# Kernel optimization log

Hardware: AMD Instinct MI355X
Metric: run time of the kernel (lower is better)

Reference implementation:

```python
import jax, jax.numpy as jnp
import numpy as np

EMB = 1024
E = 8        # num_experts
TOPK = 2
HID = 2048   # expert_dim

def setup_inputs() -> dict:
    key = jax.random.key(0)
    ks = jax.random.split(key, 10)
    s = lambda fan_in: 1.0 / np.sqrt(fan_in)
    x  = jax.random.normal(ks[0], (2, 2048, EMB), dtype=jnp.float32)
    Wr = jax.random.normal(ks[1], (EMB, E), dtype=jnp.float32) * s(EMB)
    br = jnp.zeros((E,), dtype=jnp.float32)
    # stacked expert weights, stored (in, out) so y = x @ W + b
    W1 = jax.random.normal(ks[2], (E, EMB, HID), dtype=jnp.float32) * s(EMB)
    b1 = jax.random.normal(ks[3], (E, HID), dtype=jnp.float32) * 0.01
    Wg = jax.random.normal(ks[4], (E, HID, HID), dtype=jnp.float32) * s(HID)
    bg = jax.random.normal(ks[5], (E, HID), dtype=jnp.float32) * 0.01
    W2 = jax.random.normal(ks[6], (E, HID, EMB), dtype=jnp.float32) * s(HID)
    b2 = jax.random.normal(ks[7], (E, EMB), dtype=jnp.float32) * 0.01
    return {"x": x, "Wr": Wr, "br": br, "W1": W1, "b1": b1,
            "Wg": Wg, "bg": bg, "W2": W2, "b2": b2}

def reference(x, Wr, br, W1, b1, Wg, bg, W2, b2):
    B, S, D = x.shape
    xt = x.reshape(B * S, D)                                  # [T, D]
    logits = xt @ Wr + br                                     # [T, E]
    probs = jax.nn.softmax(logits, axis=-1)
    topk_p, topk_i = jax.lax.top_k(probs, TOPK)               # [T, K]
    # dense gate matrix (top-k probs, NOT renormalized, as in source)
    gates = jnp.sum(jax.nn.one_hot(topk_i, E, dtype=xt.dtype) * topk_p[..., None], axis=1)  # [T, E]
    # expert MLP: layer1 (no act) -> relu(linear) -> layer2, for all experts
    h = jnp.einsum('td,edh->teh', xt, W1) + b1                # [T, E, HID]
    h = jax.nn.relu(jnp.einsum('teh,ehg->teg', h, Wg) + bg)   # [T, E, HID]
    y = jnp.einsum('teh,ehd->ted', h, W2) + b2                # [T, E, D]
    out = jnp.einsum('te,ted->td', gates, y)                  # weighted combine
    return out.reshape(B, S, D)
```

## Files before the change

kernel.cpp:

```cpp
#include <hip/hip_runtime.h>
#include <hip/hip_bf16.h>
#include <stdint.h>

#define NTOK 4096
#define EMBD 1024
#define NEXP 8
#define HIDD 2048
#define NPAIR (NTOK * 2)

typedef __attribute__((ext_vector_type(8))) __bf16 bf16x8;
typedef __attribute__((ext_vector_type(4))) float f32x4;

union V16 { uint4 u; bf16x8 b; };

__device__ __forceinline__ uint16_t f2bf(float f) {
    uint32_t u = __float_as_uint(f);
    return (uint16_t)((u + 0x7FFFu + ((u >> 16) & 1u)) >> 16);
}

__global__ __launch_bounds__(256) void cast_x_kernel(const float* __restrict__ x,
                                                     uint16_t* __restrict__ xb) {
    int i = blockIdx.x * 256 + threadIdx.x;
    float4 v = ((const float4*)x)[i];
    ushort4 o;
    o.x = f2bf(v.x); o.y = f2bf(v.y); o.z = f2bf(v.z); o.w = f2bf(v.w);
    ((ushort4*)xb)[i] = o;
}

__global__ __launch_bounds__(64) void router_kernel(const float* __restrict__ x,
                                                    const float* __restrict__ Wr,
                                                    const float* __restrict__ br,
                                                    int* __restrict__ counts,
                                                    int* __restrict__ pair_e,
                                                    float* __restrict__ pair_p) {
    int tok = blockIdx.x;
    int lane = threadIdx.x;
    const float* xr = x + (size_t)tok * EMBD;
    float acc[NEXP];
#pragma unroll
    for (int e = 0; e < NEXP; e++) acc[e] = 0.f;
    for (int d = lane; d < EMBD; d += 64) {
        float xv = xr[d];
#pragma unroll
        for (int e = 0; e < NEXP; e++) acc[e] += xv * Wr[d * NEXP + e];
    }
#pragma unroll
    for (int e = 0; e < NEXP; e++) {
#pragma unroll
        for (int off = 32; off > 0; off >>= 1)
            acc[e] += __shfl_down(acc[e], off, 64);
    }
    if (lane == 0) {
        float lg[NEXP];
#pragma unroll
        for (int e = 0; e < NEXP; e++) lg[e] = acc[e] + br[e];
        int e0 = 0;
#pragma unroll
        for (int e = 1; e < NEXP; e++) if (lg[e] > lg[e0]) e0 = e;
        int e1 = (e0 == 0) ? 1 : 0;
#pragma unroll
        for (int e = 0; e < NEXP; e++) if (e != e0 && lg[e] > lg[e1]) e1 = e;
        float mx = lg[0];
#pragma unroll
        for (int e = 1; e < NEXP; e++) mx = fmaxf(mx, lg[e]);
        float s = 0.f, p[NEXP];
#pragma unroll
        for (int e = 0; e < NEXP; e++) { p[e] = __expf(lg[e] - mx); s += p[e]; }
        float inv = 1.f / s;
        pair_e[tok * 2 + 0] = e0; pair_p[tok * 2 + 0] = p[e0] * inv;
        pair_e[tok * 2 + 1] = e1; pair_p[tok * 2 + 1] = p[e1] * inv;
        atomicAdd(&counts[e0], 1);
        atomicAdd(&counts[e1], 1);
    }
}

__global__ void scan_kernel(const int* __restrict__ counts, int* __restrict__ offsets) {
    if (threadIdx.x == 0 && blockIdx.x == 0) {
        int s = 0;
        for (int e = 0; e < NEXP; e++) { offsets[e] = s; s += counts[e]; }
    }
}

__global__ __launch_bounds__(256) void scatter_kernel(const int* __restrict__ pair_e,
                                                      const float* __restrict__ pair_p,
                                                      const int* __restrict__ offsets,
                                                      int* __restrict__ cursors,
                                                      int* __restrict__ toklist,
                                                      float* __restrict__ problist) {
    int i = blockIdx.x * 256 + threadIdx.x;
    int e = pair_e[i];
    int pos = offsets[e] + atomicAdd(&cursors[e], 1);
    toklist[pos] = i >> 1;
    problist[pos] = pair_p[i];
}

template <int KDIM, int NDIM, bool GATHER_A, bool RELU, bool SCATTER>
__global__ __launch_bounds__(256) void gemm_kernel(
    const uint16_t* __restrict__ Abase, const float* __restrict__ Wbase,
    const float* __restrict__ bbase, uint16_t* __restrict__ Obf,
    float* __restrict__ Oscat, const int* __restrict__ counts,
    const int* __restrict__ offsets, const int* __restrict__ toklist,
    const float* __restrict__ problist) {
    int e = blockIdx.z;
    int n_e = counts[e];
    int m0 = blockIdx.y * 64;
    if (m0 >= n_e) return;
    int n0 = blockIdx.x * 64;
    int offs = offsets[e];
    const float* W = Wbase + (size_t)e * KDIM * NDIM;
    const float* bias = bbase + (size_t)e * NDIM;

    __shared__ uint16_t As[64][40];
    __shared__ uint16_t Bs[64][40];

    int tid = threadIdx.x;
    int lane = tid & 63;
    int wave = tid >> 6;
    int wm = (wave >> 1) * 32, wn = (wave & 1) * 32;
    int qd = lane >> 4;
    int l16 = lane & 15;

    int ar = tid >> 2;
    int aseg = (tid & 3) * 8;
    bool avalid = (m0 + ar) < n_e;
    int arow;
    if (GATHER_A) {
        int p = offs + m0 + (avalid ? ar : 0);
        arow = toklist[p];
    } else {
        arow = offs + m0 + (avalid ? ar : 0);
    }
    const uint16_t* Arow = Abase + (size_t)arow * KDIM + aseg;

    int bn = tid & 63;
    int bkg = (tid >> 6) * 8;

    f32x4 acc[2][2];
    f32x4 zero = {0.f, 0.f, 0.f, 0.f};
    acc[0][0] = zero; acc[0][1] = zero; acc[1][0] = zero; acc[1][1] = zero;

    for (int kb = 0; kb < KDIM; kb += 32) {
        uint4 av = {0u, 0u, 0u, 0u};
        if (avalid) av = *(const uint4*)(Arow + kb);
        *(uint4*)(&As[ar][aseg]) = av;
#pragma unroll
        for (int kk = 0; kk < 8; kk++) {
            float bv = W[(size_t)(kb + bkg + kk) * NDIM + n0 + bn];
            Bs[bn][bkg + kk] = f2bf(bv);
        }
        __syncthreads();
        V16 afr[2], bfr[2];
#pragma unroll
        for (int t = 0; t < 2; t++) {
            afr[t].u = *(const uint4*)(&As[wm + t * 16 + l16][qd * 8]);
            bfr[t].u = *(const uint4*)(&Bs[wn + t * 16 + l16][qd * 8]);
        }
#pragma unroll
        for (int ti = 0; ti < 2; ti++)
#pragma unroll
            for (int tj = 0; tj < 2; tj++)
                acc[ti][tj] = __builtin_amdgcn_mfma_f32_16x16x32_bf16(
                    afr[ti].b, bfr[tj].b, acc[ti][tj], 0, 0, 0);
        __syncthreads();
    }

#pragma unroll
    for (int ti = 0; ti < 2; ti++) {
        int rbase = m0 + wm + ti * 16 + qd * 4;
#pragma unroll
        for (int tj = 0; tj < 2; tj++) {
            int col = n0 + wn + tj * 16 + l16;
            float bv = bias[col];
#pragma unroll
            for (int r = 0; r < 4; r++) {
                int row = rbase + r;
                if (row < n_e) {
                    float v = acc[ti][tj][r] + bv;
                    if (RELU) v = fmaxf(v, 0.f);
                    if (SCATTER) {
                        int p = offs + row;
                        int tok = toklist[p];
                        float pr = problist[p];
                        atomicAdd(&Oscat[(size_t)tok * NDIM + col], pr * v);
                    } else {
                        Obf[(size_t)(offs + row) * NDIM + col] = f2bf(v);
                    }
                }
            }
        }
    }
}

extern "C" void kernel_launch(void* const* d_in, const int* in_sizes, int n_in,
                              void* d_out, int out_size, void* d_ws, size_t ws_size,
                              hipStream_t stream) {
    const float* x  = (const float*)d_in[0];
    const float* Wr = (const float*)d_in[1];
    const float* br = (const float*)d_in[2];
    const float* W1 = (const float*)d_in[3];
    const float* b1 = (const float*)d_in[4];
    const float* Wg = (const float*)d_in[5];
    const float* bg = (const float*)d_in[6];
    const float* W2 = (const float*)d_in[7];
    const float* b2 = (const float*)d_in[8];
    float* out = (float*)d_out;

    char* ws = (char*)d_ws;
    uint16_t* xb = (uint16_t*)ws;
    uint16_t* h  = (uint16_t*)(ws + (8ull << 20));
    uint16_t* g  = (uint16_t*)(ws + (40ull << 20));
    int* meta = (int*)(ws + (72ull << 20));
    int*   counts   = meta;
    int*   offsets  = meta + 8;
    int*   cursors  = meta + 16;
    int*   pair_e   = meta + 24;
    int*   toklist  = meta + 24 + NPAIR;
    float* pair_p   = (float*)(meta + 24 + 2 * NPAIR);
    float* problist = (float*)(meta + 24 + 3 * NPAIR);

    hipMemsetAsync(out, 0, (size_t)NTOK * EMBD * sizeof(float), stream);
    hipMemsetAsync(counts, 0, 24 * sizeof(int), stream);

    cast_x_kernel<<<(NTOK * EMBD) / (256 * 4), 256, 0, stream>>>(x, xb);
    router_kernel<<<NTOK, 64, 0, stream>>>(x, Wr, br, counts, pair_e, pair_p);
    scan_kernel<<<1, 64, 0, stream>>>(counts, offsets);
    scatter_kernel<<<NPAIR / 256, 256, 0, stream>>>(pair_e, pair_p, offsets, cursors,
                                                    toklist, problist);
    gemm_kernel<EMBD, HIDD, true, false, false>
        <<<dim3(HIDD / 64, NTOK / 64, NEXP), 256, 0, stream>>>(
            xb, W1, b1, h, nullptr, counts, offsets, toklist, problist);
    gemm_kernel<HIDD, HIDD, false, true, false>
        <<<dim3(HIDD / 64, NTOK / 64, NEXP), 256, 0, stream>>>(
            h, Wg, bg, g, nullptr, counts, offsets, toklist, problist);
    gemm_kernel<HIDD, EMBD, false, false, true>
        <<<dim3(EMBD / 64, NTOK / 64, NEXP), 256, 0, stream>>>(
            g, W2, b2, nullptr, out, counts, offsets, toklist, problist);
}
```

Baseline: 858.9 us.

## Pre-transpose weights to bf16, enlarge GEMM tiles, use direct LDS loads, replace atomics with combine

Adds a transcast kernel that converts each expert's weights to bf16 in transposed (N,K) layout, so the GEMM B loads become contiguous 16-byte global_load_lds transfers into XOR-swizzled shared memory. GEMM tiles grow from 64x64 to 128x128, with 4x4 MFMA tiles per wave for more reuse. The last GEMM writes bf16 per-pair outputs, and a separate combine kernel does the weighted sum per token, replacing the fp32 atomicAdd scatter and the output memset. In exchange, every call re-reads and transposes all fp32 weights (about 200 MB), and the extra bf16 rounding of the final expert outputs may add error.

```diff
diff --git a/kernel.cpp b/kernel.cpp
--- a/kernel.cpp
+++ b/kernel.cpp
@@ -16,6 +16,14 @@
 __device__ __forceinline__ uint16_t f2bf(float f) {
     uint32_t u = __float_as_uint(f);
     return (uint16_t)((u + 0x7FFFu + ((u >> 16) & 1u)) >> 16);
+}
+__device__ __forceinline__ float bf2f(uint16_t u) {
+    return __uint_as_float(((uint32_t)u) << 16);
+}
+__device__ __forceinline__ void gl_lds16(const uint16_t* g, uint16_t* l) {
+    __builtin_amdgcn_global_load_lds(
+        (const __attribute__((address_space(1))) void*)g,
+        (__attribute__((address_space(3))) void*)l, 16, 0, 0);
 }
 
 __global__ __launch_bounds__(256) void cast_x_kernel(const float* __restrict__ x,
@@ -25,6 +33,27 @@
     ushort4 o;
     o.x = f2bf(v.x); o.y = f2bf(v.y); o.z = f2bf(v.z); o.w = f2bf(v.w);
     ((ushort4*)xb)[i] = o;
+}
+
+__global__ __launch_bounds__(256) void transcast_kernel(const float* __restrict__ src,
+                                                        uint16_t* __restrict__ dst,
+                                                        int K, int N) {
+    int e = blockIdx.z;
+    int k0 = blockIdx.y * 64, n0 = blockIdx.x * 64;
+    __shared__ uint16_t tile[64][65];
+    const float* S = src + ((size_t)e * K + k0) * N + n0;
+    uint16_t* D = dst + ((size_t)e * N + n0) * K + k0;
+    int tx = threadIdx.x & 63, ty = threadIdx.x >> 6;
+#pragma unroll
+    for (int kk = ty; kk < 64; kk += 4)
+        tile[kk][tx] = f2bf(S[(size_t)kk * N + tx]);
+    __syncthreads();
+    int tx2 = threadIdx.x & 31, tyw = threadIdx.x >> 5;
+#pragma unroll
+    for (int nn = tyw; nn < 64; nn += 8) {
+        uint32_t lo = tile[2 * tx2][nn], hi = tile[2 * tx2 + 1][nn];
+        *(uint32_t*)&D[(size_t)nn * K + 2 * tx2] = lo | (hi << 16);
+    }
 }
 
 __global__ __launch_bounds__(64) void router_kernel(const float* __restrict__ x,
@@ -82,113 +111,140 @@
 }
 
 __global__ __launch_bounds__(256) void scatter_kernel(const int* __restrict__ pair_e,
-                                                      const float* __restrict__ pair_p,
                                                       const int* __restrict__ offsets,
                                                       int* __restrict__ cursors,
                                                       int* __restrict__ toklist,
-                                                      float* __restrict__ problist) {
+                                                      int* __restrict__ posmap) {
     int i = blockIdx.x * 256 + threadIdx.x;
     int e = pair_e[i];
     int pos = offsets[e] + atomicAdd(&cursors[e], 1);
     toklist[pos] = i >> 1;
-    problist[pos] = pair_p[i];
-}
-
-template <int KDIM, int NDIM, bool GATHER_A, bool RELU, bool SCATTER>
+    posmap[i] = pos;
+}
+
+template <int KDIM, int NDIM, bool GATHER_A, bool RELU>
 __global__ __launch_bounds__(256) void gemm_kernel(
-    const uint16_t* __restrict__ Abase, const float* __restrict__ Wbase,
-    const float* __restrict__ bbase, uint16_t* __restrict__ Obf,
-    float* __restrict__ Oscat, const int* __restrict__ counts,
-    const int* __restrict__ offsets, const int* __restrict__ toklist,
-    const float* __restrict__ problist) {
+    const uint16_t* __restrict__ Abase, const uint16_t* __restrict__ Btbase,
+    const float* __restrict__ bbase, uint16_t* __restrict__ Out,
+    const int* __restrict__ counts, const int* __restrict__ offsets,
+    const int* __restrict__ toklist) {
     int e = blockIdx.z;
     int n_e = counts[e];
-    int m0 = blockIdx.y * 64;
+    int m0 = blockIdx.y * 128;
     if (m0 >= n_e) return;
-    int n0 = blockIdx.x * 64;
+    int n0 = blockIdx.x * 128;
     int offs = offsets[e];
-    const float* W = Wbase + (size_t)e * KDIM * NDIM;
-    const float* bias = bbase + (size_t)e * NDIM;
-
-    __shared__ uint16_t As[64][40];
-    __shared__ uint16_t Bs[64][40];
+    const uint16_t* Bt = Btbase + (size_t)e * NDIM * KDIM;
+
+    __shared__ uint16_t As[128 * 32];
+    __shared__ uint16_t Bs[128 * 32];
 
     int tid = threadIdx.x;
     int lane = tid & 63;
     int wave = tid >> 6;
-    int wm = (wave >> 1) * 32, wn = (wave & 1) * 32;
-    int qd = lane >> 4;
-    int l16 = lane & 15;
-
-    int ar = tid >> 2;
-    int aseg = (tid & 3) * 8;
-    bool avalid = (m0 + ar) < n_e;
-    int arow;
-    if (GATHER_A) {
-        int p = offs + m0 + (avalid ? ar : 0);
-        arow = toklist[p];
-    } else {
-        arow = offs + m0 + (avalid ? ar : 0);
-    }
-    const uint16_t* Arow = Abase + (size_t)arow * KDIM + aseg;
-
-    int bn = tid & 63;
-    int bkg = (tid >> 6) * 8;
-
-    f32x4 acc[2][2];
+
+    int sr = tid >> 2;
+    int ss = tid & 3;
+    const uint16_t* arp[2];
+    const uint16_t* brp[2];
+#pragma unroll
+    for (int p = 0; p < 2; p++) {
+        int r = p * 64 + sr;
+        int gs = ss ^ ((r >> 1) & 3);
+        int grow;
+        if (GATHER_A) {
+            int idx = m0 + r;
+            if (idx >= n_e) idx = 0;
+            grow = toklist[offs + idx];
+        } else {
+            grow = offs + m0 + r;
+        }
+        arp[p] = Abase + (size_t)grow * KDIM + gs * 8;
+        brp[p] = Bt + (size_t)(n0 + r) * KDIM + gs * 8;
+    }
+    uint16_t* alds[2] = { &As[wave * 512], &As[2048 + wave * 512] };
+    uint16_t* blds[2] = { &Bs[wave * 512], &Bs[2048 + wave * 512] };
+
+    int wm = (wave >> 1) * 64;
+    int wn = (wave & 1) * 64;
+    int l16 = lane & 15, qd = lane >> 4;
+    const uint16_t* afp[4];
+    const uint16_t* bfp[4];
+#pragma unroll
+    for (int t = 0; t < 4; t++) {
+        int ar = wm + t * 16 + l16;
+        afp[t] = &As[ar * 32 + (qd ^ ((ar >> 1) & 3)) * 8];
+        int br = wn + t * 16 + l16;
+        bfp[t] = &Bs[br * 32 + (qd ^ ((br >> 1) & 3)) * 8];
+    }
+
+    f32x4 acc[4][4];
     f32x4 zero = {0.f, 0.f, 0.f, 0.f};
-    acc[0][0] = zero; acc[0][1] = zero; acc[1][0] = zero; acc[1][1] = zero;
+#pragma unroll
+    for (int i = 0; i < 4; i++)
+#pragma unroll
+        for (int j = 0; j < 4; j++) acc[i][j] = zero;
 
     for (int kb = 0; kb < KDIM; kb += 32) {
-        uint4 av = {0u, 0u, 0u, 0u};
-        if (avalid) av = *(const uint4*)(Arow + kb);
-        *(uint4*)(&As[ar][aseg]) = av;
-#pragma unroll
-        for (int kk = 0; kk < 8; kk++) {
-            float bv = W[(size_t)(kb + bkg + kk) * NDIM + n0 + bn];
-            Bs[bn][bkg + kk] = f2bf(bv);
+#pragma unroll
+        for (int p = 0; p < 2; p++) {
+            gl_lds16(arp[p] + kb, alds[p]);
+            gl_lds16(brp[p] + kb, blds[p]);
         }
         __syncthreads();
-        V16 afr[2], bfr[2];
-#pragma unroll
-        for (int t = 0; t < 2; t++) {
-            afr[t].u = *(const uint4*)(&As[wm + t * 16 + l16][qd * 8]);
-            bfr[t].u = *(const uint4*)(&Bs[wn + t * 16 + l16][qd * 8]);
+        V16 af[4], bf[4];
+#pragma unroll
+        for (int t = 0; t < 4; t++) {
+            af[t].u = *(const uint4*)(afp[t]);
+            bf[t].u = *(const uint4*)(bfp[t]);
         }
 #pragma unroll
-        for (int ti = 0; ti < 2; ti++)
-#pragma unroll
-            for (int tj = 0; tj < 2; tj++)
-                acc[ti][tj] = __builtin_amdgcn_mfma_f32_16x16x32_bf16(
-                    afr[ti].b, bfr[tj].b, acc[ti][tj], 0, 0, 0);
+        for (int i = 0; i < 4; i++)
+#pragma unroll
+            for (int j = 0; j < 4; j++)
+                acc[i][j] = __builtin_amdgcn_mfma_f32_16x16x32_bf16(
+                    af[i].b, bf[j].b, acc[i][j], 0, 0, 0);
         __syncthreads();
     }
 
-#pragma unroll
-    for (int ti = 0; ti < 2; ti++) {
-        int rbase = m0 + wm + ti * 16 + qd * 4;
-#pragma unroll
-        for (int tj = 0; tj < 2; tj++) {
-            int col = n0 + wn + tj * 16 + l16;
+    const float* bias = bbase + (size_t)e * NDIM;
+    int mrem = n_e - m0;
+#pragma unroll
+    for (int i = 0; i < 4; i++) {
+        int rb = wm + i * 16 + qd * 4;
+#pragma unroll
+        for (int j = 0; j < 4; j++) {
+            int col = n0 + wn + j * 16 + l16;
             float bv = bias[col];
 #pragma unroll
             for (int r = 0; r < 4; r++) {
-                int row = rbase + r;
-                if (row < n_e) {
-                    float v = acc[ti][tj][r] + bv;
+                int lr = rb + r;
+                if (lr < mrem) {
+                    float v = acc[i][j][r] + bv;
                     if (RELU) v = fmaxf(v, 0.f);
-                    if (SCATTER) {
-                        int p = offs + row;
-                        int tok = toklist[p];
-                        float pr = problist[p];
-                        atomicAdd(&Oscat[(size_t)tok * NDIM + col], pr * v);
-                    } else {
-                        Obf[(size_t)(offs + row) * NDIM + col] = f2bf(v);
-                    }
+                    Out[(size_t)(offs + m0 + lr) * NDIM + col] = f2bf(v);
                 }
             }
         }
     }
+}
+
+__global__ __launch_bounds__(256) void combine_kernel(const uint16_t* __restrict__ y,
+                                                      const int* __restrict__ posmap,
+                                                      const float* __restrict__ pair_p,
+                                                      float* __restrict__ out) {
+    int t = blockIdx.x;
+    int d4 = threadIdx.x;
+    int p0 = posmap[t * 2], p1 = posmap[t * 2 + 1];
+    float w0 = pair_p[t * 2], w1 = pair_p[t * 2 + 1];
+    ushort4 a = ((const ushort4*)(y + (size_t)p0 * EMBD))[d4];
+    ushort4 b = ((const ushort4*)(y + (size_t)p1 * EMBD))[d4];
+    float4 o;
+    o.x = w0 * bf2f(a.x) + w1 * bf2f(b.x);
+    o.y = w0 * bf2f(a.y) + w1 * bf2f(b.y);
+    o.z = w0 * bf2f(a.z) + w1 * bf2f(b.z);
+    o.w = w0 * bf2f(a.w) + w1 * bf2f(b.w);
+    ((float4*)(out + (size_t)t * EMBD))[d4] = o;
 }
 
 extern "C" void kernel_launch(void* const* d_in, const int* in_sizes, int n_in,
@@ -206,33 +262,40 @@
     float* out = (float*)d_out;
 
     char* ws = (char*)d_ws;
-    uint16_t* xb = (uint16_t*)ws;
-    uint16_t* h  = (uint16_t*)(ws + (8ull << 20));
-    uint16_t* g  = (uint16_t*)(ws + (40ull << 20));
-    int* meta = (int*)(ws + (72ull << 20));
-    int*   counts   = meta;
-    int*   offsets  = meta + 8;
-    int*   cursors  = meta + 16;
-    int*   pair_e   = meta + 24;
-    int*   toklist  = meta + 24 + NPAIR;
-    float* pair_p   = (float*)(meta + 24 + 2 * NPAIR);
-    float* problist = (float*)(meta + 24 + 3 * NPAIR);
-
-    hipMemsetAsync(out, 0, (size_t)NTOK * EMBD * sizeof(float), stream);
+    uint16_t* xb  = (uint16_t*)ws;
+    uint16_t* h   = (uint16_t*)(ws + (8ull << 20));
+    uint16_t* yb  = h;
+    uint16_t* W1t = (uint16_t*)(ws + (40ull << 20));
+    uint16_t* g   = W1t;
+    uint16_t* Wgt = (uint16_t*)(ws + (72ull << 20));
+    uint16_t* W2t = (uint16_t*)(ws + (136ull << 20));
+    int* meta = (int*)(ws + (168ull << 20));
+    int*   counts  = meta;
+    int*   offsets = meta + 8;
+    int*   cursors = meta + 16;
+    int*   pair_e  = meta + 24;
+    int*   toklist = meta + 24 + NPAIR;
+    int*   posmap  = meta + 24 + 2 * NPAIR;
+    float* pair_p  = (float*)(meta + 24 + 3 * NPAIR);
+
     hipMemsetAsync(counts, 0, 24 * sizeof(int), stream);
 
     cast_x_kernel<<<(NTOK * EMBD) / (256 * 4), 256, 0, stream>>>(x, xb);
+    transcast_kernel<<<dim3(HIDD / 64, EMBD / 64, NEXP), 256, 0, stream>>>(W1, W1t, EMBD, HIDD);
+    transcast_kernel<<<dim3(HIDD / 64, HIDD / 64, NEXP), 256, 0, stream>>>(Wg, Wgt, HIDD, HIDD);
+    transcast_kernel<<<dim3(EMBD / 64, HIDD / 64, NEXP), 256, 0, stream>>>(W2, W2t, HIDD, EMBD);
     router_kernel<<<NTOK, 64, 0, stream>>>(x, Wr, br, counts, pair_e, pair_p);
     scan_kernel<<<1, 64, 0, stream>>>(counts, offsets);
-    scatter_kernel<<<NPAIR / 256, 256, 0, stream>>>(pair_e, pair_p, offsets, cursors,
-                                                    toklist, problist);
-    gemm_kernel<EMBD, HIDD, true, false, false>
-        <<<dim3(HIDD / 64, NTOK / 64, NEXP), 256, 0, stream>>>(
-            xb, W1, b1, h, nullptr, counts, offsets, toklist, problist);
-    gemm_kernel<HIDD, HIDD, false, true, false>
-        <<<dim3(HIDD / 64, NTOK / 64, NEXP), 256, 0, stream>>>(
-            h, Wg, bg, g, nullptr, counts, offsets, toklist, problist);
-    gemm_kernel<HIDD, EMBD, false, false, true>
-        <<<dim3(EMBD / 64, NTOK / 64, NEXP), 256, 0, stream>>>(
-            g, W2, b2, nullptr, out, counts, offsets, toklist, problist);
-}
+    scatter_kernel<<<NPAIR / 256, 256, 0, stream>>>(pair_e, offsets, cursors, toklist, posmap);
+
+    gemm_kernel<EMBD, HIDD, true, false>
+        <<<dim3(HIDD / 128, NTOK / 128, NEXP), 256, 0, stream>>>(
+            xb, W1t, b1, h, counts, offsets, toklist);
+    gemm_kernel<HIDD, HIDD, false, true>
+        <<<dim3(HIDD / 128, NTOK / 128, NEXP), 256, 0, stream>>>(
+            h, Wgt, bg, g, counts, offsets, toklist);
+    gemm_kernel<HIDD, EMBD, false, false>
+        <<<dim3(EMBD / 128, NTOK / 128, NEXP), 256, 0, stream>>>(
+            g, W2t, b2, yb, counts, offsets, toklist);
+    combine_kernel<<<NTOK, 256, 0, stream>>>(yb, posmap, pair_p, out);
+}
```

Measured after the change: 765.9 us. 10.8% less time.
